# Performance work log

Hardware: AMD Instinct MI355X
Metric: run time of the kernel (lower is better)

The kernel has to match this reference:

```python
import jax, jax.numpy as jnp
import numpy as np

B, CIN, COUT, K, KN, HID, HW = 16, 256, 256, 3, 4, 16, 64
PAD = K // 2
EPS = 1e-5


def setup_inputs() -> dict:
    key = jax.random.key(0)
    ks = jax.random.split(key, 6)
    x = jax.random.normal(ks[0], (B, CIN, HW, HW), dtype=jnp.float32)
    # attention MLP: 1x1 conv -> BN -> ReLU -> 1x1 conv (on 1x1 pooled maps == dense)
    w1 = jax.random.normal(ks[1], (HID, CIN), dtype=jnp.float32) * (1.0 / np.sqrt(CIN))
    bn_gamma = jnp.ones((HID,), dtype=jnp.float32)
    bn_beta = jnp.zeros((HID,), dtype=jnp.float32)
    bn_mean = jnp.zeros((HID,), dtype=jnp.float32)
    bn_var = jnp.ones((HID,), dtype=jnp.float32)
    w2 = jax.random.normal(ks[2], (KN, HID), dtype=jnp.float32) * (1.0 / np.sqrt(HID))
    # kaiming-normal fan_out: std = sqrt(2 / (Cout * k * k))
    weight = jax.random.normal(ks[3], (KN, COUT, CIN, K, K), dtype=jnp.float32) * np.sqrt(2.0 / (COUT * K * K))
    return {"x": x, "w1": w1, "bn_gamma": bn_gamma, "bn_beta": bn_beta,
            "bn_mean": bn_mean, "bn_var": bn_var, "w2": w2, "weight": weight}


def reference(x, w1, bn_gamma, bn_beta, bn_mean, bn_var, w2, weight):
    b = x.shape[0]
    # global average pool -> [B, Cin]
    pooled = jnp.mean(x, axis=(2, 3))
    h = pooled @ w1.T                                   # [B, HID]
    h = (h - bn_mean) * jax.lax.rsqrt(bn_var + EPS) * bn_gamma + bn_beta
    h = jax.nn.relu(h)
    att = jax.nn.softmax(h @ w2.T, axis=1)              # [B, KN]
    # aggregate per-sample kernels: [B, Cout, Cin, K, K]
    agg_w = jnp.einsum('bk,koijl->boijl', att, weight)
    # batched dynamic conv via batch-as-groups grouped conv
    x_g = x.reshape(1, b * CIN, x.shape[2], x.shape[3])
    w_g = agg_w.reshape(b * COUT, CIN, K, K)
    out = jax.lax.conv_general_dilated(
        x_g, w_g, window_strides=(1, 1), padding=[(PAD, PAD), (PAD, PAD)],
        dimension_numbers=('NCHW', 'OIHW', 'NCHW'), feature_group_count=b)
    return out.reshape(b, COUT, out.shape[2], out.shape[3])
```

## Files before the change

### kernel.cpp

```cpp
#include <hip/hip_runtime.h>

typedef __attribute__((ext_vector_type(8))) short bf16x8;
typedef __attribute__((ext_vector_type(4))) float f32x4;

#define AS3 __attribute__((address_space(3)))
#define AS1 __attribute__((address_space(1)))

__device__ __forceinline__ unsigned short f2bf(float f) {
  unsigned u = __float_as_uint(f);
  u += 0x7fffu + ((u >> 16) & 1u);
  return (unsigned short)(u >> 16);
}
__device__ __forceinline__ float bf2f(unsigned short v) {
  return __uint_as_float((unsigned)v << 16);
}

__global__ void transpose_kernel(const float* __restrict__ x,
                                 unsigned short* __restrict__ xTp) {
  __shared__ unsigned short tb[64][258];
  const int blk = blockIdx.x;
  const int b = blk >> 6, y = blk & 63;
  const int t = threadIdx.x;
  const int l = t & 63, w = t >> 6;
  const int coff = l >> 4;
  const int x4 = (l & 15) << 2;
  const float* src = x + (size_t)b * 256 * 4096 + (size_t)y * 64;
#pragma unroll 4
  for (int i = 0; i < 16; ++i) {
    const int c = w * 64 + i * 4 + coff;
    const float4 v = *reinterpret_cast<const float4*>(&src[(size_t)c * 4096 + x4]);
    tb[x4 + 0][c] = f2bf(v.x);
    tb[x4 + 1][c] = f2bf(v.y);
    tb[x4 + 2][c] = f2bf(v.z);
    tb[x4 + 3][c] = f2bf(v.w);
  }
  __syncthreads();
  unsigned short* dst = xTp + (size_t)b * (4356 * 256) + ((size_t)(y + 1) * 66 + 1) * 256;
#pragma unroll 4
  for (int i = 0; i < 16; ++i) {
    const int xx = w * 16 + i;
    ushort2 v0 = *(const ushort2*)&tb[xx][l * 4];
    ushort2 v1 = *(const ushort2*)&tb[xx][l * 4 + 2];
    ushort4 v = {v0.x, v0.y, v1.x, v1.y};
    *(ushort4*)&dst[(size_t)xx * 256 + l * 4] = v;
  }
}

__global__ void border_kernel(unsigned short* __restrict__ xTp) {
  const int br = blockIdx.x;
  const int b = blockIdx.y;
  int y, xx;
  if (br < 66) { y = 0; xx = br; }
  else if (br < 132) { y = 65; xx = br - 66; }
  else { const int k = br - 132; y = 1 + (k >> 1); xx = (k & 1) * 65; }
  xTp[((size_t)b * 4356 + y * 66 + xx) * 256 + threadIdx.x] = 0;
}

__global__ void pool2_kernel(const unsigned short* __restrict__ xTp,
                             float* __restrict__ pooled) {
  __shared__ float red[8][256];
  const int b = blockIdx.x;
  const int ych = blockIdx.y;
  const int t = threadIdx.x;
  const int rg = t >> 5;
  const int c8 = (t & 31) << 3;
  const unsigned short* base = xTp + (size_t)b * (4356 * 256);
  float s[8];
#pragma unroll
  for (int k = 0; k < 8; ++k) s[k] = 0.f;
  for (int rr = 0; rr < 32; ++rr) {
    const int r = rr * 8 + rg;
    const int y = ych * 4 + (r >> 6);
    const int xx = r & 63;
    const unsigned short* row =
        base + ((size_t)(y + 1) * 66 + 1 + xx) * 256 + c8;
    bf16x8 v = *reinterpret_cast<const bf16x8*>(row);
#pragma unroll
    for (int k = 0; k < 8; ++k) s[k] += bf2f((unsigned short)v[k]);
  }
#pragma unroll
  for (int k = 0; k < 8; ++k) red[rg][c8 + k] = s[k];
  __syncthreads();
  float tot = 0.f;
#pragma unroll
  for (int g = 0; g < 8; ++g) tot += red[g][t];
  atomicAdd(&pooled[b * 256 + t], tot * (1.0f / 4096.0f));
}

__global__ void attn_kernel(const float* __restrict__ pooled,
                            const float* __restrict__ w1,
                            const float* __restrict__ bng,
                            const float* __restrict__ bnb,
                            const float* __restrict__ bnm,
                            const float* __restrict__ bnv,
                            const float* __restrict__ w2,
                            float* __restrict__ att) {
  __shared__ float hbuf[256];
  const int t = threadIdx.x;
  const int b = t >> 4, i = t & 15;
  float s = 0.f;
  for (int c = 0; c < 256; ++c) s += pooled[b * 256 + c] * w1[i * 256 + c];
  float h = (s - bnm[i]) * rsqrtf(bnv[i] + 1e-5f) * bng[i] + bnb[i];
  hbuf[t] = fmaxf(h, 0.f);
  __syncthreads();
  if (t < 64) {
    const int bb = t >> 2, k = t & 3;
    float l = 0.f;
    for (int j = 0; j < 16; ++j) l += hbuf[bb * 16 + j] * w2[k * 16 + j];
    float m = l;
    m = fmaxf(m, __shfl_xor(m, 1, 64));
    m = fmaxf(m, __shfl_xor(m, 2, 64));
    float e = expf(l - m);
    float sum = e;
    sum += __shfl_xor(sum, 1, 64);
    sum += __shfl_xor(sum, 2, 64);
    att[bb * 4 + k] = e / sum;
  }
}

__global__ void agg_kernel(const float* __restrict__ att,
                           const float* __restrict__ wgt,
                           unsigned short* __restrict__ agg) {
  const int o = blockIdx.x;
  const int bh = blockIdx.y;
  const int c = threadIdx.x;
  float w[4][9];
#pragma unroll
  for (int k = 0; k < 4; ++k) {
    const float* wp = wgt + ((size_t)((k << 8) + o) * 256 + c) * 9;
#pragma unroll
    for (int t = 0; t < 9; ++t) w[k][t] = wp[t];
  }
  __shared__ float attS[64];
  if (c < 64) attS[c] = att[c];
  __syncthreads();
#pragma unroll 1
  for (int b = bh * 8; b < bh * 8 + 8; ++b) {
    const float a0 = attS[b * 4 + 0], a1 = attS[b * 4 + 1];
    const float a2 = attS[b * 4 + 2], a3 = attS[b * 4 + 3];
#pragma unroll
    for (int t = 0; t < 9; ++t) {
      const float v = a0 * w[0][t] + a1 * w[1][t] + a2 * w[2][t] + a3 * w[3][t];
      agg[(((size_t)(b * 9 + t) * 256) + o) * 256 + c] = f2bf(v);
    }
  }
}

__global__ __launch_bounds__(256, 2) void conv_kernel(
    const unsigned short* __restrict__ xTp,
    const unsigned short* __restrict__ agg,
    float* __restrict__ out) {
  __shared__ unsigned short lds[448 * 32 + 4 * 128 * 32];
  AS3 char* ldsA3 = (AS3 char*)lds;
  AS3 char* ldsB3 = ((AS3 char*)lds) + 28672;

  const int bid = blockIdx.x;
  const int b = bid & 15;
  const int rest = bid >> 4;
  const int mt = rest >> 1;
  const int nh = rest & 1;
  const int p0 = mt << 8;
  const int rowA0 = mt * 264;

  const int tid = threadIdx.x;
  const int lane = tid & 63;
  const int wave = tid >> 6;
  const int wm = wave >> 1;
  const int wn = wave & 1;

  const int srow = tid >> 2;
  const int scol = ((tid & 3) ^ ((tid >> 3) & 3)) << 3;
  const int sdst = srow * 64 + (tid & 3) * 16;

  const unsigned short* xbs =
      xTp + (size_t)b * (4356 * 256) + (size_t)rowA0 * 256 + scol;
  const unsigned short* aggs =
      agg + ((size_t)(b * 9) * 256 + nh * 128 + srow) * 256 + scol;

  auto stageA = [&](int c0) {
#pragma unroll
    for (int i = 0; i < 7; ++i) {
      const int h = srow + (i << 6);
      const int hs = h > 395 ? 395 : h;
      __builtin_amdgcn_global_load_lds(
          (const AS1 void*)(xbs + (size_t)hs * 256 + c0 * 32),
          (AS3 void*)(ldsA3 + sdst + (i << 12)), 16, 0, 0);
    }
  };
  auto stageB = [&](int c02, int tap2, int slot) {
#pragma unroll
    for (int j = 0; j < 2; ++j) {
      __builtin_amdgcn_global_load_lds(
          (const AS1 void*)(aggs + tap2 * 65536 + (j << 14) + c02 * 32),
          (AS3 void*)(ldsB3 + slot * 8192 + sdst + (j << 12)), 16, 0, 0);
    }
  };

  const int l15 = lane & 15;
  const int lhi = lane >> 4;
  const int hb0 = wm * 132 + l15;
  const int rslotB = (lhi ^ ((l15 >> 1) & 3)) << 4;
  int boffs[4];
#pragma unroll
  for (int n = 0; n < 4; ++n)
    boffs[n] = 28672 + (wn * 64 + n * 16 + l15) * 64 + rslotB;

  f32x4 acc[8][4];
#pragma unroll
  for (int m = 0; m < 8; ++m)
#pragma unroll
    for (int n = 0; n < 4; ++n) acc[m][n] = (f32x4){0.f, 0.f, 0.f, 0.f};

  stageB(0, 0, 0);
  stageB(0, 1, 1);

#pragma unroll 1
  for (int c0 = 0; c0 < 8; ++c0) {
    __builtin_amdgcn_s_barrier();
    stageA(c0);
    asm volatile("s_waitcnt vmcnt(0)" ::: "memory");
    __builtin_amdgcn_s_barrier();
#pragma unroll
    for (int tap = 0; tap < 9; ++tap) {
      if (tap != 0) {
        asm volatile("s_waitcnt vmcnt(2)" ::: "memory");
        __builtin_amdgcn_s_barrier();
      }
      __builtin_amdgcn_sched_barrier(0);
      const int dy = tap / 3, dx = tap % 3;
      const int slotR = (c0 + tap) & 3;
      bf16x8 af[8], bfr[4];
#pragma unroll
      for (int m = 0; m < 8; ++m) {
        const int h = hb0 + ((m >> 2) + dy) * 66 + (m & 3) * 16 + dx;
        const int ab = h * 64 + ((lhi ^ ((h >> 1) & 3)) << 4);
        af[m] = *(const bf16x8*)((const char*)lds + ab);
      }
#pragma unroll
      for (int n = 0; n < 4; ++n)
        bfr[n] = *(const bf16x8*)((const char*)lds + slotR * 8192 + boffs[n]);
      int c02, tap2;
      if (tap <= 6) { c02 = c0; tap2 = tap + 2; }
      else { c02 = c0 + 1; tap2 = tap - 7; }
      if (c02 > 7) { c02 = 7; tap2 = 8; }
      stageB(c02, tap2, (c0 + tap + 2) & 3);
      __builtin_amdgcn_s_setprio(1);
#pragma unroll
      for (int m = 0; m < 8; ++m)
#pragma unroll
        for (int n = 0; n < 4; ++n)
          acc[m][n] = __builtin_amdgcn_mfma_f32_16x16x32_bf16(af[m], bfr[n],
                                                              acc[m][n], 0, 0, 0);
      __builtin_amdgcn_s_setprio(0);
    }
  }

#pragma unroll
  for (int m = 0; m < 8; ++m) {
    const int p = p0 + wm * 128 + (m >> 2) * 64 + (m & 3) * 16 + (lhi << 2);
#pragma unroll
    for (int n = 0; n < 4; ++n) {
      const int co = nh * 128 + wn * 64 + n * 16 + l15;
      float* dst = out + ((size_t)(b * 256 + co) << 12) + p;
      *reinterpret_cast<f32x4*>(dst) = acc[m][n];
    }
  }
}

extern "C" void kernel_launch(void* const* d_in, const int* in_sizes, int n_in,
                              void* d_out, int out_size, void* d_ws, size_t ws_size,
                              hipStream_t stream) {
  const float* x = (const float*)d_in[0];
  const float* w1 = (const float*)d_in[1];
  const float* bng = (const float*)d_in[2];
  const float* bnb = (const float*)d_in[3];
  const float* bnm = (const float*)d_in[4];
  const float* bnv = (const float*)d_in[5];
  const float* w2 = (const float*)d_in[6];
  const float* wgt = (const float*)d_in[7];
  float* out = (float*)d_out;

  char* ws = (char*)d_ws;
  const size_t xtp_bytes = (size_t)16 * 4356 * 256 * 2;
  const size_t agg_bytes = (size_t)16 * 9 * 256 * 256 * 2;
  unsigned short* xTp = (unsigned short*)ws;
  unsigned short* agg = (unsigned short*)(ws + xtp_bytes);
  float* pooled = (float*)(ws + xtp_bytes + agg_bytes);
  float* att = (float*)(ws + xtp_bytes + agg_bytes + 16384);

  hipMemsetAsync(pooled, 0, 16 * 256 * sizeof(float), stream);
  border_kernel<<<dim3(260, 16), 256, 0, stream>>>(xTp);
  transpose_kernel<<<1024, 256, 0, stream>>>(x, xTp);
  pool2_kernel<<<dim3(16, 16), 256, 0, stream>>>(xTp, pooled);
  attn_kernel<<<1, 256, 0, stream>>>(pooled, w1, bng, bnb, bnm, bnv, w2, att);
  agg_kernel<<<dim3(256, 2), 256, 0, stream>>>(att, wgt, agg);
  conv_kernel<<<512, 256, 0, stream>>>(xTp, agg, out);
}
```

Measured before the change: 121.2 us.

## Fuse pooling and padding into transpose, double-buffer conv fragments, deepen B prefetch

Folds the global-average-pool partial sums and the zero-border writes into the transpose kernel. This removes the memset, border and pool2 launches and the re-read of xTp, and adds a small per-batch finalize kernel. In the conv kernel, LDS fragments for the next tap are loaded into alternate registers while the current tap's MFMAs run, and B staging prefetches three taps ahead instead of two. The extra fragment registers may lower occupancy. Four B slots with a prefetch distance of three leave only a thin margin against overwriting a slot that is still being read.

```diff
diff --git a/kernel.cpp b/kernel.cpp
--- a/kernel.cpp
+++ b/kernel.cpp
@@ -16,8 +16,10 @@
 }
 
 __global__ void transpose_kernel(const float* __restrict__ x,
-                                 unsigned short* __restrict__ xTp) {
+                                 unsigned short* __restrict__ xTp,
+                                 float* __restrict__ part) {
   __shared__ unsigned short tb[64][258];
+  __shared__ float redf[4][256];
   const int blk = blockIdx.x;
   const int b = blk >> 6, y = blk & 63;
   const int t = threadIdx.x;
@@ -35,56 +37,40 @@
     tb[x4 + 3][c] = f2bf(v.w);
   }
   __syncthreads();
-  unsigned short* dst = xTp + (size_t)b * (4356 * 256) + ((size_t)(y + 1) * 66 + 1) * 256;
+  unsigned short* dstb = xTp + (size_t)b * (4356 * 256);
+  unsigned short* dst = dstb + ((size_t)(y + 1) * 66 + 1) * 256;
+  float s0 = 0.f, s1 = 0.f, s2 = 0.f, s3 = 0.f;
 #pragma unroll 4
   for (int i = 0; i < 16; ++i) {
     const int xx = w * 16 + i;
     ushort2 v0 = *(const ushort2*)&tb[xx][l * 4];
     ushort2 v1 = *(const ushort2*)&tb[xx][l * 4 + 2];
+    s0 += bf2f(v0.x); s1 += bf2f(v0.y); s2 += bf2f(v1.x); s3 += bf2f(v1.y);
     ushort4 v = {v0.x, v0.y, v1.x, v1.y};
     *(ushort4*)&dst[(size_t)xx * 256 + l * 4] = v;
   }
-}
-
-__global__ void border_kernel(unsigned short* __restrict__ xTp) {
-  const int br = blockIdx.x;
-  const int b = blockIdx.y;
-  int y, xx;
-  if (br < 66) { y = 0; xx = br; }
-  else if (br < 132) { y = 65; xx = br - 66; }
-  else { const int k = br - 132; y = 1 + (k >> 1); xx = (k & 1) * 65; }
-  xTp[((size_t)b * 4356 + y * 66 + xx) * 256 + threadIdx.x] = 0;
-}
-
-__global__ void pool2_kernel(const unsigned short* __restrict__ xTp,
-                             float* __restrict__ pooled) {
-  __shared__ float red[8][256];
-  const int b = blockIdx.x;
-  const int ych = blockIdx.y;
-  const int t = threadIdx.x;
-  const int rg = t >> 5;
-  const int c8 = (t & 31) << 3;
-  const unsigned short* base = xTp + (size_t)b * (4356 * 256);
-  float s[8];
-#pragma unroll
-  for (int k = 0; k < 8; ++k) s[k] = 0.f;
-  for (int rr = 0; rr < 32; ++rr) {
-    const int r = rr * 8 + rg;
-    const int y = ych * 4 + (r >> 6);
-    const int xx = r & 63;
-    const unsigned short* row =
-        base + ((size_t)(y + 1) * 66 + 1 + xx) * 256 + c8;
-    bf16x8 v = *reinterpret_cast<const bf16x8*>(row);
-#pragma unroll
-    for (int k = 0; k < 8; ++k) s[k] += bf2f((unsigned short)v[k]);
-  }
-#pragma unroll
-  for (int k = 0; k < 8; ++k) red[rg][c8 + k] = s[k];
+  redf[w][l * 4 + 0] = s0;
+  redf[w][l * 4 + 1] = s1;
+  redf[w][l * 4 + 2] = s2;
+  redf[w][l * 4 + 3] = s3;
+  unsigned short* rowpad = dstb + ((size_t)(y + 1) * 66) * 256;
+  rowpad[t] = 0;
+  rowpad[65 * 256 + t] = 0;
+  if (y == 0)
+    for (int xx = 0; xx < 66; ++xx) dstb[(size_t)xx * 256 + t] = 0;
+  if (y == 63)
+    for (int xx = 0; xx < 66; ++xx) dstb[(size_t)(65 * 66 + xx) * 256 + t] = 0;
   __syncthreads();
-  float tot = 0.f;
-#pragma unroll
-  for (int g = 0; g < 8; ++g) tot += red[g][t];
-  atomicAdd(&pooled[b * 256 + t], tot * (1.0f / 4096.0f));
+  part[((size_t)(b * 64 + y)) * 256 + t] =
+      redf[0][t] + redf[1][t] + redf[2][t] + redf[3][t];
+}
+
+__global__ void poolfin_kernel(const float* __restrict__ part,
+                               float* __restrict__ pooled) {
+  const int b = blockIdx.x, c = threadIdx.x;
+  float s = 0.f;
+  for (int y = 0; y < 64; ++y) s += part[((size_t)(b * 64 + y)) * 256 + c];
+  pooled[b * 256 + c] = s * (1.0f / 4096.0f);
 }
 
 __global__ void attn_kernel(const float* __restrict__ pooled,
@@ -211,48 +197,71 @@
 #pragma unroll
     for (int n = 0; n < 4; ++n) acc[m][n] = (f32x4){0.f, 0.f, 0.f, 0.f};
 
+#define LDFRAG(AF, BF, tap)                                                   \
+  {                                                                           \
+    const int dy_ = (tap) / 3, dx_ = (tap) % 3;                               \
+    const int slotR_ = (c0 + (tap)) & 3;                                      \
+    _Pragma("unroll") for (int m = 0; m < 8; ++m) {                           \
+      const int h_ = hb0 + ((m >> 2) + dy_) * 66 + (m & 3) * 16 + dx_;        \
+      AF[m] = *(const bf16x8*)((const char*)lds + h_ * 64 +                   \
+                               ((lhi ^ ((h_ >> 1) & 3)) << 4));               \
+    }                                                                         \
+    _Pragma("unroll") for (int n = 0; n < 4; ++n) {                           \
+      BF[n] = *(const bf16x8*)((const char*)lds + slotR_ * 8192 + boffs[n]);  \
+    }                                                                         \
+  }
+
+#define STAGEBT(t)                                                \
+  {                                                               \
+    int c02_, tap2_;                                              \
+    if ((t) <= 5) { c02_ = c0; tap2_ = (t) + 3; }                 \
+    else { c02_ = c0 + 1; tap2_ = (t) - 6; }                      \
+    if (c02_ > 7) { c02_ = 7; tap2_ = 8; }                        \
+    stageB(c02_, tap2_, (c0 + (t) + 3) & 3);                      \
+  }
+
+#define MFMACL(AF, BF)                                                        \
+  _Pragma("unroll") for (int m = 0; m < 8; ++m)                               \
+  _Pragma("unroll") for (int n = 0; n < 4; ++n)                               \
+      acc[m][n] =                                                             \
+          __builtin_amdgcn_mfma_f32_16x16x32_bf16(AF[m], BF[n], acc[m][n], 0, 0, 0);
+
+#define TAPITER(t, AFc, BFc, AFn, BFn, PREF)                         \
+  {                                                                  \
+    if ((t) > 0) {                                                   \
+      asm volatile("s_waitcnt vmcnt(2)" ::: "memory");               \
+      __builtin_amdgcn_s_barrier();                                  \
+      __builtin_amdgcn_sched_barrier(0);                             \
+    }                                                                \
+    STAGEBT(t);                                                      \
+    if (PREF) LDFRAG(AFn, BFn, (t) + 1);                             \
+    __builtin_amdgcn_s_setprio(1);                                   \
+    MFMACL(AFc, BFc);                                                \
+    __builtin_amdgcn_s_setprio(0);                                   \
+  }
+
   stageB(0, 0, 0);
   stageB(0, 1, 1);
+  stageB(0, 2, 2);
 
 #pragma unroll 1
   for (int c0 = 0; c0 < 8; ++c0) {
+    bf16x8 afr0[8], afr1[8], bfr0[4], bfr1[4];
     __builtin_amdgcn_s_barrier();
     stageA(c0);
     asm volatile("s_waitcnt vmcnt(0)" ::: "memory");
     __builtin_amdgcn_s_barrier();
-#pragma unroll
-    for (int tap = 0; tap < 9; ++tap) {
-      if (tap != 0) {
-        asm volatile("s_waitcnt vmcnt(2)" ::: "memory");
-        __builtin_amdgcn_s_barrier();
-      }
-      __builtin_amdgcn_sched_barrier(0);
-      const int dy = tap / 3, dx = tap % 3;
-      const int slotR = (c0 + tap) & 3;
-      bf16x8 af[8], bfr[4];
-#pragma unroll
-      for (int m = 0; m < 8; ++m) {
-        const int h = hb0 + ((m >> 2) + dy) * 66 + (m & 3) * 16 + dx;
-        const int ab = h * 64 + ((lhi ^ ((h >> 1) & 3)) << 4);
-        af[m] = *(const bf16x8*)((const char*)lds + ab);
-      }
-#pragma unroll
-      for (int n = 0; n < 4; ++n)
-        bfr[n] = *(const bf16x8*)((const char*)lds + slotR * 8192 + boffs[n]);
-      int c02, tap2;
-      if (tap <= 6) { c02 = c0; tap2 = tap + 2; }
-      else { c02 = c0 + 1; tap2 = tap - 7; }
-      if (c02 > 7) { c02 = 7; tap2 = 8; }
-      stageB(c02, tap2, (c0 + tap + 2) & 3);
-      __builtin_amdgcn_s_setprio(1);
-#pragma unroll
-      for (int m = 0; m < 8; ++m)
-#pragma unroll
-        for (int n = 0; n < 4; ++n)
-          acc[m][n] = __builtin_amdgcn_mfma_f32_16x16x32_bf16(af[m], bfr[n],
-                                                              acc[m][n], 0, 0, 0);
-      __builtin_amdgcn_s_setprio(0);
-    }
+    __builtin_amdgcn_sched_barrier(0);
+    LDFRAG(afr0, bfr0, 0);
+    TAPITER(0, afr0, bfr0, afr1, bfr1, 1);
+    TAPITER(1, afr1, bfr1, afr0, bfr0, 1);
+    TAPITER(2, afr0, bfr0, afr1, bfr1, 1);
+    TAPITER(3, afr1, bfr1, afr0, bfr0, 1);
+    TAPITER(4, afr0, bfr0, afr1, bfr1, 1);
+    TAPITER(5, afr1, bfr1, afr0, bfr0, 1);
+    TAPITER(6, afr0, bfr0, afr1, bfr1, 1);
+    TAPITER(7, afr1, bfr1, afr0, bfr0, 1);
+    TAPITER(8, afr0, bfr0, afr1, bfr1, 0);
   }
 
 #pragma unroll
@@ -287,11 +296,10 @@
   unsigned short* agg = (unsigned short*)(ws + xtp_bytes);
   float* pooled = (float*)(ws + xtp_bytes + agg_bytes);
   float* att = (float*)(ws + xtp_bytes + agg_bytes + 16384);
-
-  hipMemsetAsync(pooled, 0, 16 * 256 * sizeof(float), stream);
-  border_kernel<<<dim3(260, 16), 256, 0, stream>>>(xTp);
-  transpose_kernel<<<1024, 256, 0, stream>>>(x, xTp);
-  pool2_kernel<<<dim3(16, 16), 256, 0, stream>>>(xTp, pooled);
+  float* part = (float*)(ws + xtp_bytes + agg_bytes + 20480);
+
+  transpose_kernel<<<1024, 256, 0, stream>>>(x, xTp, part);
+  poolfin_kernel<<<16, 256, 0, stream>>>(part, pooled);
   attn_kernel<<<1, 256, 0, stream>>>(pooled, w1, bng, bnb, bnm, bnv, w2, att);
   agg_kernel<<<dim3(256, 2), 256, 0, stream>>>(att, wgt, agg);
   conv_kernel<<<512, 256, 0, stream>>>(xTp, agg, out);
```

New measurement: 123.0 us. No clear change (+1.5%).

## Fuse pooling and border zeroing into transpose kernel, drop memset and pool pass

Applied to the files above, without the earlier changes.

The transpose kernel now accumulates per-row channel sums from its LDS tile and writes per-block partial sums, and it zeroes the padding border itself. A small poolfin kernel reduces these partials deterministically, replacing the memset, border_kernel and pool2_kernel, which removes a full re-read of the bf16 transposed tensor and three launches. The conv kernel also gains an s_sleep stall on half of its blocks, which looks like a scheduling experiment that adds idle time to those blocks.

```diff
diff --git a/kernel.cpp b/kernel.cpp
--- a/kernel.cpp
+++ b/kernel.cpp
@@ -16,8 +16,10 @@
 }
 
 __global__ void transpose_kernel(const float* __restrict__ x,
-                                 unsigned short* __restrict__ xTp) {
+                                 unsigned short* __restrict__ xTp,
+                                 float* __restrict__ part) {
   __shared__ unsigned short tb[64][258];
+  __shared__ float redf[4][256];
   const int blk = blockIdx.x;
   const int b = blk >> 6, y = blk & 63;
   const int t = threadIdx.x;
@@ -35,56 +37,40 @@
     tb[x4 + 3][c] = f2bf(v.w);
   }
   __syncthreads();
-  unsigned short* dst = xTp + (size_t)b * (4356 * 256) + ((size_t)(y + 1) * 66 + 1) * 256;
+  unsigned short* dstb = xTp + (size_t)b * (4356 * 256);
+  unsigned short* dst = dstb + ((size_t)(y + 1) * 66 + 1) * 256;
+  float s0 = 0.f, s1 = 0.f, s2 = 0.f, s3 = 0.f;
 #pragma unroll 4
   for (int i = 0; i < 16; ++i) {
     const int xx = w * 16 + i;
     ushort2 v0 = *(const ushort2*)&tb[xx][l * 4];
     ushort2 v1 = *(const ushort2*)&tb[xx][l * 4 + 2];
+    s0 += bf2f(v0.x); s1 += bf2f(v0.y); s2 += bf2f(v1.x); s3 += bf2f(v1.y);
     ushort4 v = {v0.x, v0.y, v1.x, v1.y};
     *(ushort4*)&dst[(size_t)xx * 256 + l * 4] = v;
   }
-}
-
-__global__ void border_kernel(unsigned short* __restrict__ xTp) {
-  const int br = blockIdx.x;
-  const int b = blockIdx.y;
-  int y, xx;
-  if (br < 66) { y = 0; xx = br; }
-  else if (br < 132) { y = 65; xx = br - 66; }
-  else { const int k = br - 132; y = 1 + (k >> 1); xx = (k & 1) * 65; }
-  xTp[((size_t)b * 4356 + y * 66 + xx) * 256 + threadIdx.x] = 0;
-}
-
-__global__ void pool2_kernel(const unsigned short* __restrict__ xTp,
-                             float* __restrict__ pooled) {
-  __shared__ float red[8][256];
-  const int b = blockIdx.x;
-  const int ych = blockIdx.y;
-  const int t = threadIdx.x;
-  const int rg = t >> 5;
-  const int c8 = (t & 31) << 3;
-  const unsigned short* base = xTp + (size_t)b * (4356 * 256);
-  float s[8];
-#pragma unroll
-  for (int k = 0; k < 8; ++k) s[k] = 0.f;
-  for (int rr = 0; rr < 32; ++rr) {
-    const int r = rr * 8 + rg;
-    const int y = ych * 4 + (r >> 6);
-    const int xx = r & 63;
-    const unsigned short* row =
-        base + ((size_t)(y + 1) * 66 + 1 + xx) * 256 + c8;
-    bf16x8 v = *reinterpret_cast<const bf16x8*>(row);
-#pragma unroll
-    for (int k = 0; k < 8; ++k) s[k] += bf2f((unsigned short)v[k]);
-  }
-#pragma unroll
-  for (int k = 0; k < 8; ++k) red[rg][c8 + k] = s[k];
-  __syncthreads();
-  float tot = 0.f;
-#pragma unroll
-  for (int g = 0; g < 8; ++g) tot += red[g][t];
-  atomicAdd(&pooled[b * 256 + t], tot * (1.0f / 4096.0f));
+  redf[w][l * 4 + 0] = s0;
+  redf[w][l * 4 + 1] = s1;
+  redf[w][l * 4 + 2] = s2;
+  redf[w][l * 4 + 3] = s3;
+  unsigned short* rowpad = dstb + ((size_t)(y + 1) * 66) * 256;
+  rowpad[t] = 0;
+  rowpad[65 * 256 + t] = 0;
+  if (y == 0)
+    for (int xx = 0; xx < 66; ++xx) dstb[(size_t)xx * 256 + t] = 0;
+  if (y == 63)
+    for (int xx = 0; xx < 66; ++xx) dstb[(size_t)(65 * 66 + xx) * 256 + t] = 0;
+  __syncthreads();
+  part[((size_t)(b * 64 + y)) * 256 + t] =
+      redf[0][t] + redf[1][t] + redf[2][t] + redf[3][t];
+}
+
+__global__ void poolfin_kernel(const float* __restrict__ part,
+                               float* __restrict__ pooled) {
+  const int b = blockIdx.x, c = threadIdx.x;
+  float s = 0.f;
+  for (int y = 0; y < 64; ++y) s += part[((size_t)(b * 64 + y)) * 256 + c];
+  pooled[b * 256 + c] = s * (1.0f / 4096.0f);
 }
 
 __global__ void attn_kernel(const float* __restrict__ pooled,
@@ -155,6 +141,12 @@
   AS3 char* ldsB3 = ((AS3 char*)lds) + 28672;
 
   const int bid = blockIdx.x;
+
+  if ((bid >> 8) & 1) {
+    __builtin_amdgcn_s_sleep(8);
+    __builtin_amdgcn_s_sleep(8);
+  }
+
   const int b = bid & 15;
   const int rest = bid >> 4;
   const int mt = rest >> 1;
@@ -287,11 +279,10 @@
   unsigned short* agg = (unsigned short*)(ws + xtp_bytes);
   float* pooled = (float*)(ws + xtp_bytes + agg_bytes);
   float* att = (float*)(ws + xtp_bytes + agg_bytes + 16384);
-
-  hipMemsetAsync(pooled, 0, 16 * 256 * sizeof(float), stream);
-  border_kernel<<<dim3(260, 16), 256, 0, stream>>>(xTp);
-  transpose_kernel<<<1024, 256, 0, stream>>>(x, xTp);
-  pool2_kernel<<<dim3(16, 16), 256, 0, stream>>>(xTp, pooled);
+  float* part = (float*)(ws + xtp_bytes + agg_bytes + 20480);
+
+  transpose_kernel<<<1024, 256, 0, stream>>>(x, xTp, part);
+  poolfin_kernel<<<16, 256, 0, stream>>>(part, pooled);
   attn_kernel<<<1, 256, 0, stream>>>(pooled, w1, bng, bnb, bnm, bnv, w2, att);
   agg_kernel<<<dim3(256, 2), 256, 0, stream>>>(att, wgt, agg);
   conv_kernel<<<512, 256, 0, stream>>>(xTp, agg, out);
```

Result: faster. 110.7 us (-8.7%).
